# Kernel optimization log

Hardware: AMD Instinct MI355X
Metric: run time of the kernel (lower is better)

Reference implementation:

```python
import jax, jax.numpy as jnp
import numpy as np

VOCAB, EMB, HID, T, B = 10000, 1500, 1500, 35, 64
FORGET_BIAS = 1.0

def setup_inputs() -> dict:
    key = jax.random.key(0)
    ks = jax.random.split(key, 8)
    s = 0.02
    return {
        'x': jax.random.randint(ks[0], (T, B), 0, VOCAB),
        'y': jax.random.randint(ks[1], (T, B), 0, VOCAB),
        'embedding': jax.random.normal(ks[2], (VOCAB, EMB), jnp.float32) * s,
        'W0': jax.random.normal(ks[3], (EMB + HID, 4 * HID), jnp.float32) * s,
        'b0': jnp.zeros((4 * HID,), jnp.float32),
        'W1': jax.random.normal(ks[4], (2 * HID, 4 * HID), jnp.float32) * s,
        'b1': jnp.zeros((4 * HID,), jnp.float32),
        'softmax_w': jax.random.normal(ks[5], (HID, VOCAB), jnp.float32) * 0.1,
        'softmax_b': jnp.zeros((VOCAB,), jnp.float32),
    }

def _lstm_step(c, h, x, W, b):
    # TF LSTMCell: z = [x, h] @ W + b; gate order i, j, f, o; forget_bias added to f
    z = jnp.concatenate([x, h], axis=-1) @ W + b
    i, j, f, o = jnp.split(z, 4, axis=-1)
    c_new = c * jax.nn.sigmoid(f + FORGET_BIAS) + jax.nn.sigmoid(i) * jnp.tanh(j)
    h_new = jnp.tanh(c_new) * jax.nn.sigmoid(o)
    return c_new, h_new

def reference(x, y, embedding, W0, b0, W1, b1, softmax_w, softmax_b):
    inputs = embedding[x]  # [T, B, EMB] (time_major)
    zeros = jnp.zeros((B, HID), inputs.dtype)
    init = (zeros, zeros, zeros, zeros)  # (c0, h0, c1, h1)

    def step(carry, xt):
        c0, h0, c1, h1 = carry
        c0, h0 = _lstm_step(c0, h0, xt, W0, b0)
        c1, h1 = _lstm_step(c1, h1, h0, W1, b1)
        return (c0, h0, c1, h1), h1

    _, outputs = jax.lax.scan(step, init, inputs)  # [T, B, HID]
    logits = outputs.reshape(-1, HID) @ softmax_w + softmax_b  # [T*B, VOCAB]
    logp = jax.nn.log_softmax(logits, axis=-1)
    tgt = y.reshape(-1)
    nll = -jnp.take_along_axis(logp, tgt[:, None], axis=-1)[:, 0]
    loss = jnp.sum(nll) / B  # sequence_loss_by_example with unit weights, / batch_size
    return loss
```

## Files before the change

### kernel.cpp

```cpp
#include <hip/hip_runtime.h>
#include <math.h>

#define TT 35
#define BB 64
#define EMB 1500
#define HID 1500
#define VOCAB 10000
#define KT 3072
#define KG 768
#define NCH 24
#define KLP 1504
#define NBLK 158
#define MROWS 2240
#define MPAD 2304
#define LBLK 94
#define FORGET_BIAS 1.0f

typedef __bf16 bf16x8 __attribute__((ext_vector_type(8)));
typedef float f32x4 __attribute__((ext_vector_type(4)));

__device__ __forceinline__ unsigned short f2bf(float f) {
    unsigned int u = __builtin_bit_cast(unsigned int, f);
    u += 0x7fffu + ((u >> 16) & 1u);
    return (unsigned short)(u >> 16);
}
__device__ __forceinline__ float sigmoidf_(float x) { return 1.0f / (1.0f + expf(-x)); }

#define GLOAD_LDS16(gp, lp) __builtin_amdgcn_global_load_lds( \
    (const __attribute__((address_space(1))) void*)(gp),      \
    (__attribute__((address_space(3))) void*)(lp), 16, 0, 0)

__global__ __launch_bounds__(256) void convT(const float* __restrict__ W,
                                             unsigned short* __restrict__ WT,
                                             int K, int N, int KP) {
    __shared__ float tile[32][33];
    int tx = threadIdx.x, ty = threadIdx.y;
    int n0 = blockIdx.x * 32, k0 = blockIdx.y * 32;
#pragma unroll
    for (int i = 0; i < 4; ++i) {
        int k = k0 + ty + 8 * i, n = n0 + tx;
        tile[ty + 8 * i][tx] = (k < K && n < N) ? W[(size_t)k * N + n] : 0.f;
    }
    __syncthreads();
#pragma unroll
    for (int i = 0; i < 4; ++i) {
        int n = n0 + ty + 8 * i, k = k0 + tx;
        if (n < N) WT[(size_t)n * KP + k] = f2bf(tile[tx][ty + 8 * i]);
    }
}

__global__ __launch_bounds__(256) void embed_kernel(const int* __restrict__ x,
                                                    const float* __restrict__ emb,
                                                    unsigned short* __restrict__ A0) {
    int tok = blockIdx.x;
    int v = x[tok];
    const float* src = emb + (size_t)v * EMB;
    unsigned short* dst = A0 + (size_t)tok * KT;
    for (int i = threadIdx.x; i < EMB; i += 256) dst[i] = f2bf(src[i]);
}

__global__ __launch_bounds__(1024) void lstm_pair(
        const unsigned short* __restrict__ A_0, const unsigned short* __restrict__ WT_0,
        const float* __restrict__ bias_0, float* __restrict__ cst_0,
        unsigned short* __restrict__ d1_0, int s1_0, unsigned short* __restrict__ d2_0, int s2_0,
        const unsigned short* __restrict__ A_1, const unsigned short* __restrict__ WT_1,
        const float* __restrict__ bias_1, float* __restrict__ cst_1,
        unsigned short* __restrict__ d1_1, int s1_1, unsigned short* __restrict__ d2_1, int s2_1) {
    __shared__ __align__(16) unsigned char smem[131072];

    const unsigned short* A;  const unsigned short* WT;
    const float* bias;        float* cst;
    unsigned short* d1; int s1; unsigned short* d2; int s2;
    int nb;
    if (blockIdx.x < LBLK) {
        if (!A_0) return;
        A = A_0; WT = WT_0; bias = bias_0; cst = cst_0;
        d1 = d1_0; s1 = s1_0; d2 = d2_0; s2 = s2_0;
        nb = blockIdx.x;
    } else {
        if (!A_1) return;
        A = A_1; WT = WT_1; bias = bias_1; cst = cst_1;
        d1 = d1_1; s1 = s1_1; d2 = d2_1; s2 = s2_1;
        nb = blockIdx.x - LBLK;
    }

    int tid = threadIdx.x;
    int wv = tid >> 6, lane = tid & 63;
    int mt = wv & 3, kg = wv >> 2;
    int quad = lane >> 4, l16 = lane & 15;
    int col = nb * 16 + l16;

    int rr = lane >> 2, p = lane & 3;
    int sp = p ^ (rr & 3) ^ ((rr >> 2) & 3);
    int kbase = kg * KG;
    int q0 = mt * 2, q1 = q0 + 1;
    const unsigned short* gp[2];
    int ldsoff[2];
#pragma unroll
    for (int ii = 0; ii < 2; ++ii) {
        int q = ii ? q1 : q0;
        if (q < 4) {
            gp[ii] = A + (size_t)(16 * q + rr) * KT + kbase + sp * 8;
        } else {
            int g = q - 4;
            int ci = nb * 16 + rr; if (ci > HID - 1) ci = HID - 1;
            gp[ii] = WT + (size_t)(g * HID + ci) * KT + kbase + sp * 8;
        }
        ldsoff[ii] = ((q >> 2) * 4 + kg) * 4096 + (q & 3) * 1024;
    }

    int swz = (quad ^ (l16 & 3) ^ ((l16 >> 2) & 3)) * 16;
    int aoff = (0 * 4 + kg) * 4096 + (mt * 16 + l16) * 64 + swz;
    int boff = (1 * 4 + kg) * 4096 + l16 * 64 + swz;

    f32x4 acc0 = {0.f,0.f,0.f,0.f}, acc1 = acc0, acc2 = acc0, acc3 = acc0;

#pragma unroll
    for (int s = 0; s < 2; ++s) {
        GLOAD_LDS16(gp[0] + s * 32, smem + s * 32768 + ldsoff[0]);
        GLOAD_LDS16(gp[1] + s * 32, smem + s * 32768 + ldsoff[1]);
    }

    const int NIT = NCH / 2;
    for (int it = 0; it < NIT; ++it) {
        asm volatile("s_waitcnt vmcnt(0)" ::: "memory");
        __builtin_amdgcn_sched_barrier(0);
        __builtin_amdgcn_s_barrier();
        if (it + 1 < NIT) {
            int nb2 = ((it + 1) & 1) * 65536;
#pragma unroll
            for (int s = 0; s < 2; ++s) {
                GLOAD_LDS16(gp[0] + (2 * (it + 1) + s) * 32, smem + nb2 + s * 32768 + ldsoff[0]);
                GLOAD_LDS16(gp[1] + (2 * (it + 1) + s) * 32, smem + nb2 + s * 32768 + ldsoff[1]);
            }
        }
        const unsigned char* base = smem + (it & 1) * 65536;
#pragma unroll
        for (int s = 0; s < 2; ++s) {
            const unsigned char* bs2 = base + s * 32768;
            bf16x8 a  = *(const bf16x8*)(bs2 + aoff);
            bf16x8 b0 = *(const bf16x8*)(bs2 + boff);
            bf16x8 b1 = *(const bf16x8*)(bs2 + boff + 1024);
            bf16x8 b2 = *(const bf16x8*)(bs2 + boff + 2048);
            bf16x8 b3 = *(const bf16x8*)(bs2 + boff + 3072);
            __builtin_amdgcn_s_setprio(1);
            acc0 = __builtin_amdgcn_mfma_f32_16x16x32_bf16(a, b0, acc0, 0, 0, 0);
            acc1 = __builtin_amdgcn_mfma_f32_16x16x32_bf16(a, b1, acc1, 0, 0, 0);
            acc2 = __builtin_amdgcn_mfma_f32_16x16x32_bf16(a, b2, acc2, 0, 0, 0);
            acc3 = __builtin_amdgcn_mfma_f32_16x16x32_bf16(a, b3, acc3, 0, 0, 0);
            __builtin_amdgcn_s_setprio(0);
        }
    }
    asm volatile("s_waitcnt vmcnt(0)" ::: "memory");
    __builtin_amdgcn_sched_barrier(0);
    __syncthreads();

    float* red = (float*)smem;
    if (kg > 0) {
        int w = (kg - 1) * 4 + mt;
#pragma unroll
        for (int r = 0; r < 4; ++r) {
            red[(w * 64 + lane) * 16 + r]      = acc0[r];
            red[(w * 64 + lane) * 16 + 4 + r]  = acc1[r];
            red[(w * 64 + lane) * 16 + 8 + r]  = acc2[r];
            red[(w * 64 + lane) * 16 + 12 + r] = acc3[r];
        }
    }
    __syncthreads();
    if (kg == 0) {
#pragma unroll
        for (int k2 = 0; k2 < 3; ++k2) {
            int w = k2 * 4 + mt;
#pragma unroll
            for (int r = 0; r < 4; ++r) {
                acc0[r] += red[(w * 64 + lane) * 16 + r];
                acc1[r] += red[(w * 64 + lane) * 16 + 4 + r];
                acc2[r] += red[(w * 64 + lane) * 16 + 8 + r];
                acc3[r] += red[(w * 64 + lane) * 16 + 12 + r];
            }
        }
        if (col < HID) {
            float bi = bias[col], bj = bias[HID + col];
            float bf_ = bias[2 * HID + col], bo = bias[3 * HID + col];
#pragma unroll
            for (int r = 0; r < 4; ++r) {
                int row = mt * 16 + quad * 4 + r;
                float zi = acc0[r] + bi;
                float zj = acc1[r] + bj;
                float zf = acc2[r] + bf_;
                float zo = acc3[r] + bo;
                int ci = row * HID + col;
                float cn = cst[ci] * sigmoidf_(zf + FORGET_BIAS) + sigmoidf_(zi) * tanhf(zj);
                float hn = tanhf(cn) * sigmoidf_(zo);
                cst[ci] = cn;
                unsigned short hb = f2bf(hn);
                d1[(size_t)row * s1 + col] = hb;
                if (d2) d2[(size_t)row * s2 + col] = hb;
            }
        }
    }
}

__global__ __launch_bounds__(256) void logits_fold(const unsigned short* __restrict__ A,
                                                   const unsigned short* __restrict__ WT,
                                                   const float* __restrict__ sb,
                                                   const int* __restrict__ y,
                                                   float2* __restrict__ partials,
                                                   float* __restrict__ tgtlog) {
    __shared__ __align__(16) unsigned char smem[32768];

    int orig = blockIdx.x;
    int xcd = orig & 7, j = orig >> 3;
    int mb, bn;
    if (xcd < 7) { bn = xcd * 10 + j % 10; mb = j / 10; }
    else { if (j >= 162) return; bn = 70 + j % 9; mb = j / 9; }
    int n0 = bn * 128;

    int tid = threadIdx.x;
    int wv = tid >> 6, lane = tid & 63;
    int wr = wv >> 1, wc = wv & 1;
    int quad = lane >> 4, l16 = lane & 15;

    int rr = lane >> 2;
    int ks = (lane & 3) ^ (rr & 3);
    const unsigned short* gA[2]; const unsigned short* gB[2];
    int ldsA[2], ldsB[2];
#pragma unroll
    for (int i = 0; i < 2; ++i) {
        int r16 = wv * 2 + i;
        int ra = mb * 128 + r16 * 16 + rr;
        gA[i] = A + (size_t)ra * KLP + ks * 8;
        ldsA[i] = r16 * 1024;
        int rb = n0 + r16 * 16 + rr;
        if (rb > VOCAB - 1) rb = VOCAB - 1;
        gB[i] = WT + (size_t)rb * KLP + ks * 8;
        ldsB[i] = 8192 + r16 * 1024;
    }

    int sw16 = (quad ^ (l16 & 3)) * 16;
    int aoff[4], boff[4];
#pragma unroll
    for (int f = 0; f < 4; ++f) {
        aoff[f] = (wr * 64 + f * 16 + l16) * 64 + sw16;
        boff[f] = 8192 + (wc * 64 + f * 16 + l16) * 64 + sw16;
    }

    f32x4 acc[4][4];
#pragma unroll
    for (int i = 0; i < 4; ++i)
#pragma unroll
        for (int jj = 0; jj < 4; ++jj) acc[i][jj] = (f32x4){0.f, 0.f, 0.f, 0.f};

#pragma unroll
    for (int i = 0; i < 2; ++i) {
        GLOAD_LDS16(gA[i], smem + ldsA[i]);
        GLOAD_LDS16(gB[i], smem + ldsB[i]);
    }
    __syncthreads();

    for (int c = 0; c < KLP / 32; ++c) {
        int buf = c & 1;
        if (c + 1 < KLP / 32) {
            int ob = (buf ^ 1) * 16384;
#pragma unroll
            for (int i = 0; i < 2; ++i) {
                GLOAD_LDS16(gA[i] + (c + 1) * 32, smem + ob + ldsA[i]);
                GLOAD_LDS16(gB[i] + (c + 1) * 32, smem + ob + ldsB[i]);
            }
        }
        const unsigned char* base = smem + buf * 16384;
        bf16x8 a[4], b[4];
#pragma unroll
        for (int f = 0; f < 4; ++f) {
            a[f] = *(const bf16x8*)(base + aoff[f]);
            b[f] = *(const bf16x8*)(base + boff[f]);
        }
#pragma unroll
        for (int ar = 0; ar < 4; ++ar)
#pragma unroll
            for (int cbv = 0; cbv < 4; ++cbv)
                acc[ar][cbv] = __builtin_amdgcn_mfma_f32_16x16x32_bf16(a[ar], b[cbv], acc[ar][cbv], 0, 0, 0);
        __syncthreads();
    }

    int colv[4]; float bs[4];
#pragma unroll
    for (int cbv = 0; cbv < 4; ++cbv) {
        int c = n0 + wc * 64 + cbv * 16 + l16;
        colv[cbv] = c;
        int cc = (c < VOCAB) ? c : (VOCAB - 1);
        bs[cbv] = sb[cc];
    }
    int nb2 = bn * 2 + wc;
#pragma unroll
    for (int ar = 0; ar < 4; ++ar) {
#pragma unroll
        for (int r2 = 0; r2 < 4; ++r2) {
            float v0 = acc[ar][0][r2] + bs[0];
            float v1 = acc[ar][1][r2] + bs[1];
            float v2 = acc[ar][2][r2] + bs[2];
            float v3 = acc[ar][3][r2] + bs[3];
            if (colv[0] >= VOCAB) v0 = -1e30f;
            if (colv[1] >= VOCAB) v1 = -1e30f;
            if (colv[2] >= VOCAB) v2 = -1e30f;
            if (colv[3] >= VOCAB) v3 = -1e30f;
            int row = mb * 128 + wr * 64 + ar * 16 + quad * 4 + r2;
            int t = y[row < MROWS ? row : 0];
            float tv = -1e30f;
            if (colv[0] == t) tv = v0;
            if (colv[1] == t) tv = v1;
            if (colv[2] == t) tv = v2;
            if (colv[3] == t) tv = v3;
            float mx = fmaxf(fmaxf(v0, v1), fmaxf(v2, v3));
#pragma unroll
            for (int d = 1; d < 16; d <<= 1) mx = fmaxf(mx, __shfl_xor(mx, d, 64));
            float sum = expf(v0 - mx) + expf(v1 - mx) + expf(v2 - mx) + expf(v3 - mx);
#pragma unroll
            for (int d = 1; d < 16; d <<= 1) sum += __shfl_xor(sum, d, 64);
#pragma unroll
            for (int d = 1; d < 16; d <<= 1) tv = fmaxf(tv, __shfl_xor(tv, d, 64));
            if (l16 == 0 && row < MROWS) {
                partials[(size_t)row * NBLK + nb2] = make_float2(mx, sum);
                if (tv > -5e29f) tgtlog[row] = tv;
            }
        }
    }
}

__global__ __launch_bounds__(64) void nll_reduce(const float2* __restrict__ partials,
                                                 const float* __restrict__ tgtlog,
                                                 float* __restrict__ nll) {
    int row = blockIdx.x;
    int lane = threadIdx.x;
    float2 loc[3];
    int cnt = 0;
    float m = -1e30f;
    for (int i = lane; i < NBLK; i += 64) {
        float2 p = partials[(size_t)row * NBLK + i];
        loc[cnt++] = p;
        m = fmaxf(m, p.x);
    }
#pragma unroll
    for (int d = 1; d < 64; d <<= 1) m = fmaxf(m, __shfl_xor(m, d, 64));
    float s = 0.f;
    for (int jj = 0; jj < cnt; ++jj) s += loc[jj].y * expf(loc[jj].x - m);
#pragma unroll
    for (int d = 1; d < 64; d <<= 1) s += __shfl_xor(s, d, 64);
    if (lane == 0) nll[row] = -(tgtlog[row] - m - logf(s));
}

__global__ __launch_bounds__(256) void loss_kernel(const float* __restrict__ nll,
                                                   float* __restrict__ out) {
    __shared__ float red[256];
    int tid = threadIdx.x;
    float s = 0.f;
    for (int i = tid; i < TT * BB; i += 256) s += nll[i];
    red[tid] = s; __syncthreads();
    for (int st = 128; st > 0; st >>= 1) { if (tid < st) red[tid] += red[tid + st]; __syncthreads(); }
    if (tid == 0) out[0] = red[0] / (float)BB;
}

extern "C" void kernel_launch(void* const* d_in, const int* in_sizes, int n_in,
                              void* d_out, int out_size, void* d_ws, size_t ws_size,
                              hipStream_t stream) {
    const int*   x   = (const int*)d_in[0];
    const int*   y   = (const int*)d_in[1];
    const float* emb = (const float*)d_in[2];
    const float* W0  = (const float*)d_in[3];
    const float* b0  = (const float*)d_in[4];
    const float* W1  = (const float*)d_in[5];
    const float* b1  = (const float*)d_in[6];
    const float* sw  = (const float*)d_in[7];
    const float* sb  = (const float*)d_in[8];
    float* out = (float*)d_out;

    char* p = (char*)d_ws;
    unsigned short* A0   = (unsigned short*)p; p += (size_t)TT * BB * KT * 2;
    unsigned short* A1   = (unsigned short*)p; p += (size_t)2 * BB * KT * 2;
    unsigned short* outs = (unsigned short*)p; p += (size_t)MPAD * KLP * 2;
    float* c0 = (float*)p; p += (size_t)BB * HID * 4;
    float* c1 = (float*)p; p += (size_t)BB * HID * 4;
    size_t zero_bytes = (size_t)(p - (char*)d_ws);
    unsigned short* WbT0 = (unsigned short*)p; p += (size_t)6000 * KT * 2;
    unsigned short* WbT1 = (unsigned short*)p; p += (size_t)6000 * KT * 2;
    unsigned short* swT  = (unsigned short*)p; p += (size_t)VOCAB * KLP * 2;
    float2* partials = (float2*)p; p += (size_t)TT * BB * NBLK * 8;
    float* tgtlog = (float*)p; p += (size_t)TT * BB * 4;
    float* nll    = (float*)p;

    hipMemsetAsync(d_ws, 0, zero_bytes, stream);

    dim3 cblk(32, 8);
    convT<<<dim3(188, 96), cblk, 0, stream>>>(W0, WbT0, 3000, 6000, KT);
    convT<<<dim3(188, 96), cblk, 0, stream>>>(W1, WbT1, 3000, 6000, KT);
    convT<<<dim3(313, 47), cblk, 0, stream>>>(sw, swT, HID, VOCAB, KLP);

    embed_kernel<<<TT * BB, 256, 0, stream>>>(x, emb, A0);

    for (int k = 0; k <= TT; ++k) {
        const unsigned short* A0t = (k < TT) ? A0 + (size_t)k * BB * KT : nullptr;
        unsigned short* d1_0 = A1 + (size_t)(k & 1) * BB * KT;
        unsigned short* d2_0 = (k < TT - 1) ? (A0 + (size_t)(k + 1) * BB * KT + EMB) : nullptr;

        const unsigned short* A1t = (k >= 1) ? A1 + (size_t)((k - 1) & 1) * BB * KT : nullptr;
        unsigned short* d1_1 = A1 + (size_t)(k & 1) * BB * KT + HID;
        unsigned short* d2_1 = (k >= 1) ? outs + (size_t)(k - 1) * BB * KLP : nullptr;

        lstm_pair<<<188, 1024, 0, stream>>>(A0t, WbT0, b0, c0, d1_0, KT, d2_0, KT,
                                            A1t, WbT1, b1, c1, d1_1, KT, d2_1, KLP);
    }

    logits_fold<<<1440, 256, 0, stream>>>(outs, swT, sb, y, partials, tgtlog);
    nll_reduce<<<TT * BB, 64, 0, stream>>>(partials, tgtlog, nll);
    loss_kernel<<<1, 256, 0, stream>>>(nll, out);
}
```

Before: 1.324 ms.

## Split LSTM step blocks by batch half and use triple-buffered per-chunk pipeline

Each LSTM step launch now splits every 16-column job into two blocks covering 32 batch rows each, giving 384 blocks of 512 threads instead of 188 of 1024, with a block index mapping that places the two halves of a column job in nearby blocks. The K loop changes from double-buffered two-chunk iterations to a three-slot ring with a prefetch distance of two chunks and a partial vmcnt wait. The aim is to occupy more of the CUs per launch and overlap loads with MFMA work in this latency-bound recurrent step. In exchange, each weight tile is now fetched twice, once per batch half, which raises L2 traffic.

```diff
diff --git a/kernel.cpp b/kernel.cpp
--- a/kernel.cpp
+++ b/kernel.cpp
@@ -14,6 +14,7 @@
 #define MROWS 2240
 #define MPAD 2304
 #define LBLK 94
+#define NJOB 188
 #define FORGET_BIAS 1.0f
 
 typedef __bf16 bf16x8 __attribute__((ext_vector_type(8)));
@@ -59,97 +60,95 @@
     for (int i = threadIdx.x; i < EMB; i += 256) dst[i] = f2bf(src[i]);
 }
 
-__global__ __launch_bounds__(1024) void lstm_pair(
+__global__ __launch_bounds__(512) void lstm_pair(
         const unsigned short* __restrict__ A_0, const unsigned short* __restrict__ WT_0,
         const float* __restrict__ bias_0, float* __restrict__ cst_0,
         unsigned short* __restrict__ d1_0, int s1_0, unsigned short* __restrict__ d2_0, int s2_0,
         const unsigned short* __restrict__ A_1, const unsigned short* __restrict__ WT_1,
         const float* __restrict__ bias_1, float* __restrict__ cst_1,
         unsigned short* __restrict__ d1_1, int s1_1, unsigned short* __restrict__ d2_1, int s2_1) {
-    __shared__ __align__(16) unsigned char smem[131072];
+    __shared__ __align__(16) unsigned char smem[73728];
+
+    int b = blockIdx.x;
+    int q = 8 * (b >> 4) + (b & 7);
+    int rh = (b >> 3) & 1;
+    if (q >= NJOB) return;
 
     const unsigned short* A;  const unsigned short* WT;
     const float* bias;        float* cst;
     unsigned short* d1; int s1; unsigned short* d2; int s2;
-    int nb;
-    if (blockIdx.x < LBLK) {
+    int cb;
+    if (q < LBLK) {
         if (!A_0) return;
         A = A_0; WT = WT_0; bias = bias_0; cst = cst_0;
         d1 = d1_0; s1 = s1_0; d2 = d2_0; s2 = s2_0;
-        nb = blockIdx.x;
+        cb = q;
     } else {
         if (!A_1) return;
         A = A_1; WT = WT_1; bias = bias_1; cst = cst_1;
         d1 = d1_1; s1 = s1_1; d2 = d2_1; s2 = s2_1;
-        nb = blockIdx.x - LBLK;
+        cb = q - LBLK;
     }
 
     int tid = threadIdx.x;
     int wv = tid >> 6, lane = tid & 63;
-    int mt = wv & 3, kg = wv >> 2;
+    int mt = wv & 1, kg = wv >> 1;
     int quad = lane >> 4, l16 = lane & 15;
-    int col = nb * 16 + l16;
+    int col = cb * 16 + l16;
 
     int rr = lane >> 2, p = lane & 3;
     int sp = p ^ (rr & 3) ^ ((rr >> 2) & 3);
     int kbase = kg * KG;
-    int q0 = mt * 2, q1 = q0 + 1;
-    const unsigned short* gp[2];
-    int ldsoff[2];
-#pragma unroll
-    for (int ii = 0; ii < 2; ++ii) {
-        int q = ii ? q1 : q0;
-        if (q < 4) {
-            gp[ii] = A + (size_t)(16 * q + rr) * KT + kbase + sp * 8;
+
+    const unsigned short* gp[3];
+    int ldsoff[3];
+#pragma unroll
+    for (int ii = 0; ii < 3; ++ii) {
+        int idx = mt * 3 + ii;
+        if (idx < 2) {
+            gp[ii] = A + (size_t)(rh * 32 + 16 * idx + rr) * KT + kbase + sp * 8;
+            ldsoff[ii] = kg * 6144 + idx * 1024;
         } else {
-            int g = q - 4;
-            int ci = nb * 16 + rr; if (ci > HID - 1) ci = HID - 1;
+            int g = idx - 2;
+            int ci = cb * 16 + rr; if (ci > HID - 1) ci = HID - 1;
             gp[ii] = WT + (size_t)(g * HID + ci) * KT + kbase + sp * 8;
-        }
-        ldsoff[ii] = ((q >> 2) * 4 + kg) * 4096 + (q & 3) * 1024;
+            ldsoff[ii] = kg * 6144 + 2048 + g * 1024;
+        }
     }
 
     int swz = (quad ^ (l16 & 3) ^ ((l16 >> 2) & 3)) * 16;
-    int aoff = (0 * 4 + kg) * 4096 + (mt * 16 + l16) * 64 + swz;
-    int boff = (1 * 4 + kg) * 4096 + l16 * 64 + swz;
+    int aoff = kg * 6144 + (mt * 16 + l16) * 64 + swz;
+    int boff = kg * 6144 + 2048 + l16 * 64 + swz;
 
     f32x4 acc0 = {0.f,0.f,0.f,0.f}, acc1 = acc0, acc2 = acc0, acc3 = acc0;
 
 #pragma unroll
-    for (int s = 0; s < 2; ++s) {
-        GLOAD_LDS16(gp[0] + s * 32, smem + s * 32768 + ldsoff[0]);
-        GLOAD_LDS16(gp[1] + s * 32, smem + s * 32768 + ldsoff[1]);
-    }
-
-    const int NIT = NCH / 2;
-    for (int it = 0; it < NIT; ++it) {
-        asm volatile("s_waitcnt vmcnt(0)" ::: "memory");
+    for (int ci = 0; ci < 2; ++ci)
+#pragma unroll
+        for (int ii = 0; ii < 3; ++ii)
+            GLOAD_LDS16(gp[ii] + ci * 32, smem + ci * 24576 + ldsoff[ii]);
+
+    for (int c = 0; c < NCH; ++c) {
+        asm volatile("s_waitcnt vmcnt(3)" ::: "memory");
         __builtin_amdgcn_sched_barrier(0);
         __builtin_amdgcn_s_barrier();
-        if (it + 1 < NIT) {
-            int nb2 = ((it + 1) & 1) * 65536;
-#pragma unroll
-            for (int s = 0; s < 2; ++s) {
-                GLOAD_LDS16(gp[0] + (2 * (it + 1) + s) * 32, smem + nb2 + s * 32768 + ldsoff[0]);
-                GLOAD_LDS16(gp[1] + (2 * (it + 1) + s) * 32, smem + nb2 + s * 32768 + ldsoff[1]);
-            }
-        }
-        const unsigned char* base = smem + (it & 1) * 65536;
-#pragma unroll
-        for (int s = 0; s < 2; ++s) {
-            const unsigned char* bs2 = base + s * 32768;
-            bf16x8 a  = *(const bf16x8*)(bs2 + aoff);
-            bf16x8 b0 = *(const bf16x8*)(bs2 + boff);
-            bf16x8 b1 = *(const bf16x8*)(bs2 + boff + 1024);
-            bf16x8 b2 = *(const bf16x8*)(bs2 + boff + 2048);
-            bf16x8 b3 = *(const bf16x8*)(bs2 + boff + 3072);
-            __builtin_amdgcn_s_setprio(1);
-            acc0 = __builtin_amdgcn_mfma_f32_16x16x32_bf16(a, b0, acc0, 0, 0, 0);
-            acc1 = __builtin_amdgcn_mfma_f32_16x16x32_bf16(a, b1, acc1, 0, 0, 0);
-            acc2 = __builtin_amdgcn_mfma_f32_16x16x32_bf16(a, b2, acc2, 0, 0, 0);
-            acc3 = __builtin_amdgcn_mfma_f32_16x16x32_bf16(a, b3, acc3, 0, 0, 0);
-            __builtin_amdgcn_s_setprio(0);
-        }
+        int cs = (c + 2 < NCH) ? (c + 2) : (NCH - 1);
+        int bs_ = ((c + 2) % 3) * 24576;
+#pragma unroll
+        for (int ii = 0; ii < 3; ++ii)
+            GLOAD_LDS16(gp[ii] + cs * 32, smem + bs_ + ldsoff[ii]);
+        const unsigned char* base = smem + (c % 3) * 24576;
+        bf16x8 a  = *(const bf16x8*)(base + aoff);
+        bf16x8 b0 = *(const bf16x8*)(base + boff);
+        bf16x8 b1 = *(const bf16x8*)(base + boff + 1024);
+        bf16x8 b2 = *(const bf16x8*)(base + boff + 2048);
+        bf16x8 b3 = *(const bf16x8*)(base + boff + 3072);
+        __builtin_amdgcn_s_setprio(1);
+        acc0 = __builtin_amdgcn_mfma_f32_16x16x32_bf16(a, b0, acc0, 0, 0, 0);
+        acc1 = __builtin_amdgcn_mfma_f32_16x16x32_bf16(a, b1, acc1, 0, 0, 0);
+        acc2 = __builtin_amdgcn_mfma_f32_16x16x32_bf16(a, b2, acc2, 0, 0, 0);
+        acc3 = __builtin_amdgcn_mfma_f32_16x16x32_bf16(a, b3, acc3, 0, 0, 0);
+        __builtin_amdgcn_s_setprio(0);
     }
     asm volatile("s_waitcnt vmcnt(0)" ::: "memory");
     __builtin_amdgcn_sched_barrier(0);
@@ -157,7 +156,7 @@
 
     float* red = (float*)smem;
     if (kg > 0) {
-        int w = (kg - 1) * 4 + mt;
+        int w = (kg - 1) * 2 + mt;
 #pragma unroll
         for (int r = 0; r < 4; ++r) {
             red[(w * 64 + lane) * 16 + r]      = acc0[r];
@@ -170,7 +169,7 @@
     if (kg == 0) {
 #pragma unroll
         for (int k2 = 0; k2 < 3; ++k2) {
-            int w = k2 * 4 + mt;
+            int w = k2 * 2 + mt;
 #pragma unroll
             for (int r = 0; r < 4; ++r) {
                 acc0[r] += red[(w * 64 + lane) * 16 + r];
@@ -184,7 +183,7 @@
             float bf_ = bias[2 * HID + col], bo = bias[3 * HID + col];
 #pragma unroll
             for (int r = 0; r < 4; ++r) {
-                int row = mt * 16 + quad * 4 + r;
+                int row = rh * 32 + mt * 16 + quad * 4 + r;
                 float zi = acc0[r] + bi;
                 float zj = acc1[r] + bj;
                 float zf = acc2[r] + bf_;
@@ -406,8 +405,8 @@
         unsigned short* d1_1 = A1 + (size_t)(k & 1) * BB * KT + HID;
         unsigned short* d2_1 = (k >= 1) ? outs + (size_t)(k - 1) * BB * KLP : nullptr;
 
-        lstm_pair<<<188, 1024, 0, stream>>>(A0t, WbT0, b0, c0, d1_0, KT, d2_0, KT,
-                                            A1t, WbT1, b1, c1, d1_1, KT, d2_1, KLP);
+        lstm_pair<<<384, 512, 0, stream>>>(A0t, WbT0, b0, c0, d1_0, KT, d2_0, KT,
+                                           A1t, WbT1, b1, c1, d1_1, KT, d2_1, KLP);
     }
 
     logits_fold<<<1440, 256, 0, stream>>>(outs, swT, sb, y, partials, tgtlog);
```

Result: slower. 1.414 ms (+6.8%).
